# Kernel optimization log

Hardware: AMD Instinct MI355X
Metric: run time of the kernel (lower is better)

Reference implementation:

```python
import jax, jax.numpy as jnp
import numpy as np
from jax import lax

DN_CONV = ('NCHW', 'OIHW', 'NCHW')
DN_DECONV = ('NCHW', 'IOHW', 'NCHW')


def _conv(x, w, b, stride, pad):
    y = lax.conv_general_dilated(x, w, (stride, stride), ((pad, pad), (pad, pad)),
                                 dimension_numbers=DN_CONV)
    return y + b[None, :, None, None]


def _deconv(x, w, b):
    # torch ConvTranspose2d(k=4, stride=2, padding=1): equivalent to conv with
    # lhs_dilation=2, padding=k-1-p=2, spatially flipped kernel, weight [Cin,Cout,kH,kW].
    wf = w[:, :, ::-1, ::-1]
    y = lax.conv_general_dilated(x, wf, (1, 1), ((2, 2), (2, 2)),
                                 lhs_dilation=(2, 2), dimension_numbers=DN_DECONV)
    return y + b[None, :, None, None]


def setup_inputs() -> dict:
    key = jax.random.key(0)
    ks = jax.random.split(key, 14)
    s = 0.05
    H, D, K = 128, 64, 512  # hidden, embedding_dim, num_embeddings
    inp = {
        'x': jax.random.normal(ks[0], (32, 3, 256, 256), jnp.float32),
        'enc_w1': jax.random.normal(ks[1], (H, 3, 4, 4), jnp.float32) * s,
        'enc_b1': jnp.zeros((H,), jnp.float32),
        'enc_w2': jax.random.normal(ks[2], (H, H, 4, 4), jnp.float32) * s,
        'enc_b2': jnp.zeros((H,), jnp.float32),
        'enc_w3': jax.random.normal(ks[3], (D, H, 3, 3), jnp.float32) * s,
        'enc_b3': jnp.zeros((D,), jnp.float32),
        'codebook': jax.random.uniform(ks[4], (K, D), jnp.float32, -1.0 / K, 1.0 / K),
        'dec_w1': jax.random.normal(ks[5], (H, D, 3, 3), jnp.float32) * s,
        'dec_b1': jnp.zeros((H,), jnp.float32),
        'dec_w2': jax.random.normal(ks[6], (H, H, 4, 4), jnp.float32) * s,  # [Cin,Cout,4,4]
        'dec_b2': jnp.zeros((H,), jnp.float32),
        'dec_w3': jax.random.normal(ks[7], (H, 3, 4, 4), jnp.float32) * s,  # [Cin,Cout,4,4]
        'dec_b3': jnp.zeros((3,), jnp.float32),
    }
    return inp


def reference(x, enc_w1, enc_b1, enc_w2, enc_b2, enc_w3, enc_b3, codebook,
              dec_w1, dec_b1, dec_w2, dec_b2, dec_w3, dec_b3):
    # encoder
    h = jax.nn.relu(_conv(x, enc_w1, enc_b1, 2, 1))
    h = jax.nn.relu(_conv(h, enc_w2, enc_b2, 2, 1))
    z_e = _conv(h, enc_w3, enc_b3, 1, 1)  # [B, D, 64, 64]

    # vector quantization (faithful to torch .view(-1, D) memory reshape)
    D = codebook.shape[1]
    flat = z_e.reshape(-1, D)  # [N, D]
    d2 = (jnp.sum(flat * flat, axis=1, keepdims=True)
          + jnp.sum(codebook * codebook, axis=1)
          - 2.0 * flat @ codebook.T)  # [N, K]
    idx = jnp.argmin(d2, axis=1)
    z_q = jnp.take(codebook, idx, axis=0).reshape(z_e.shape)

    # decoder
    h = jax.nn.relu(_conv(z_q, dec_w1, dec_b1, 1, 1))
    h = jax.nn.relu(_deconv(h, dec_w2, dec_b2))
    x_recon = _deconv(h, dec_w3, dec_b3)
    return (x_recon, z_e, z_q)
```

## Files before the change

kernel.cpp:

```cpp
#include <hip/hip_runtime.h>
#include <hip/hip_bf16.h>


typedef unsigned short u16;
typedef unsigned int u32;
typedef unsigned long long u64;
typedef __attribute__((ext_vector_type(8))) short short8;
typedef __attribute__((ext_vector_type(4))) float f32x4;

__device__ __forceinline__ float bf2f(u16 u) {
    union { u32 i; float f; } x; x.i = ((u32)u) << 16; return x.f;
}
__device__ __forceinline__ u16 f2bf(float f) {
    __hip_bfloat16 h = __float2bfloat16(f);
    return *reinterpret_cast<u16*>(&h);
}

__global__ void g_k3(const float* __restrict__ w, u16* __restrict__ wg,
                     int CIN, int COUT)
{
    int idx = blockIdx.x * 256 + threadIdx.x;
    if (idx >= 9 * CIN * COUT) return;
    int ci = idx % CIN;
    int co = (idx / CIN) % COUT;
    int s  = idx / (CIN * COUT);
    wg[idx] = f2bf(w[(co * CIN + ci) * 9 + s]);
}

__global__ void g_enc2(const float* __restrict__ w, u16* __restrict__ wg)
{
    int idx = blockIdx.x * 256 + threadIdx.x;
    int ci = idx & 127, co = (idx >> 7) & 127, s = (idx >> 14) & 3, p = idx >> 16;
    int a = p >> 1, b = p & 1, j = s >> 1, i = s & 1;
    int ky = (1 - a) + 2 * j, kx = (1 - b) + 2 * i;
    wg[idx] = f2bf(w[((co << 7 | ci) << 4) + ky * 4 + kx]);
}

__global__ void g_dec2(const float* __restrict__ w, u16* __restrict__ wg)
{
    int idx = blockIdx.x * 256 + threadIdx.x;
    int ci = idx & 127, co = (idx >> 7) & 127, s = (idx >> 14) & 3, p = idx >> 16;
    int py = p >> 1, px = p & 1, j = s >> 1, i = s & 1;
    wg[idx] = f2bf(w[((ci << 7 | co) << 4) + (3 - (py + 2 * j)) * 4 + (3 - (px + 2 * i))]);
}

__global__ void g_dec3m(const float* __restrict__ w, u16* __restrict__ wg)
{
    int idx = blockIdx.x * 256 + threadIdx.x;
    if (idx >= 18432) return;
    int ci  = idx & 127;
    int row = (idx >> 7) & 15;
    int t   = idx >> 11;
    int dy = t / 3 - 1, dx = t % 3 - 1;
    float v = 0.f;
    if (row < 12) {
        int p = row / 3, co = row % 3;
        int py = p >> 1, px = p & 1;
        int a = dy + 1 - py, b2 = dx + 1 - px;
        if (a >= 0 && a <= 1 && b2 >= 0 && b2 <= 1)
            v = w[((ci * 3 + co) * 4 + (3 - (py + 2 * a))) * 4 + (3 - (px + 2 * b2))];
    }
    wg[idx] = f2bf(v);
}

__global__ void g_enc1(const float* __restrict__ w, u16* __restrict__ wg)
{
    int idx = blockIdx.x * 256 + threadIdx.x;
    if (idx >= 8192) return;
    int ci = idx & 3, kx = (idx >> 2) & 3, ky = (idx >> 4) & 3, co = idx >> 6;
    float v = 0.f;
    if (ci < 3) v = w[((co * 3 + ci) * 4 + ky) * 4 + kx];
    wg[idx] = f2bf(v);
}

__global__ void g_cbk(const float* __restrict__ cbk, u16* __restrict__ cb,
                      float* __restrict__ cn)
{
    int idx = blockIdx.x * 256 + threadIdx.x;
    if (idx >= 32768) return;
    cb[idx] = f2bf(cbk[idx]);
    if (idx < 512) {
        float s = 0.f;
        const float* r = cbk + idx * 64;
        for (int i = 0; i < 64; i++) s += r[i] * r[i];
        cn[idx] = s;
    }
}

__global__ __launch_bounds__(256) void xcl_k(
    const float* __restrict__ x, u16* __restrict__ xcl)
{
    const int y = blockIdx.x % 258, n = blockIdx.x / 258;
    const int gy = y - 1;
    for (int xx = threadIdx.x; xx < 258; xx += 256) {
        const int gx = xx - 1;
        u16 pk[4] = {0, 0, 0, 0};
        if (gy >= 0 && gy < 256 && gx >= 0 && gx < 256) {
            const size_t base = ((size_t)n * 3 * 256 + gy) * 256 + gx;
            pk[0] = f2bf(x[base]);
            pk[1] = f2bf(x[base + 65536]);
            pk[2] = f2bf(x[base + 131072]);
        }
        *(u64*)(xcl + ((size_t)(n * 258 + y) * 258 + xx) * 4) = *(const u64*)pk;
    }
}

__global__ __launch_bounds__(256) void enc1m_k(
    const u16* __restrict__ xcl, const u16* __restrict__ wg,
    const float* __restrict__ bias, u16* __restrict__ P)
{
    const int tid = threadIdx.x;
    const int l = tid & 63, w = tid >> 6;
    const int ln = l & 15, kg = l >> 4;
    const int px = w >> 1, half = w & 1;

    const int oy = blockIdx.x & 127;
    const int n  = blockIdx.x >> 7;
    const int p  = (oy & 1) * 2 + px;
    const int yy = oy >> 1;

    short8 af[8][2];
#pragma unroll
    for (int u = 0; u < 8; u++)
#pragma unroll
        for (int s = 0; s < 2; s++)
            af[u][s] = *(const short8*)(wg + ((u * 16 + ln) << 6) + s * 32 + 8 * kg);

    const u16* xn = xcl + (size_t)n * 258 * 258 * 4;
    const int r0 = 2 * oy;

#pragma unroll
    for (int t = 0; t < 2; t++) {
        const int xq = half * 32 + t * 16 + ln;
        const int ox = px + 2 * xq;

        short8 bf[2];
#pragma unroll
        for (int s = 0; s < 2; s++) {
            const int row = r0 + 2 * s + (kg >> 1);
            bf[s] = *(const short8*)(xn + ((size_t)row * 258 + 2 * ox) * 4
                                     + (kg & 1) * 8);
        }

        f32x4 acc[8];
#pragma unroll
        for (int u = 0; u < 8; u++) acc[u] = (f32x4){0.f, 0.f, 0.f, 0.f};
#pragma unroll
        for (int u = 0; u < 8; u++) {
            acc[u] = __builtin_amdgcn_mfma_f32_16x16x32_bf16(af[u][0], bf[0], acc[u], 0, 0, 0);
            acc[u] = __builtin_amdgcn_mfma_f32_16x16x32_bf16(af[u][1], bf[1], acc[u], 0, 0, 0);
        }

#pragma unroll
        for (int u = 0; u < 8; u++) {
            const int cobase = u * 16 + 4 * kg;
            u16 pk[4];
#pragma unroll
            for (int r = 0; r < 4; r++)
                pk[r] = f2bf(fmaxf(acc[u][r] + bias[cobase + r], 0.f));
            *(u64*)(P + ((((size_t)(n * 4 + p) * 64 + yy) * 64 + xq) << 7) + cobase)
                = *(const u64*)pk;
        }
    }
}

template<int J, int I, int NP, int NCW, int CI, int OUTM>
__global__ __launch_bounds__(512) void conv_mx3(
    const u16* __restrict__ x, const u16* __restrict__ wg,
    const float* __restrict__ bias, void* __restrict__ yv,
    int COUT)
{
    constexpr int G = 8 / NCW;
    constexpr int RS = 2 * G + 2;
    constexpr int TASKS = RS * 68 * 4;
    constexpr int SLOTS = (TASKS + 511) / 512;
    constexpr int CHP = CI / 32;
    constexpr int NCHUNK = NP * CHP;
    __shared__ u16 XL[RS * 68 * 40];

    const int tid = threadIdx.x;
    const int l = tid & 63, wv = tid >> 6;
    const int kg = l >> 4, ln = l & 15;
    const int cw = wv % NCW, g = wv / NCW;

    int b = blockIdx.x;
    constexpr int TILES = 64 / (2 * G);
    const int tile = b % TILES;  b /= TILES;
    const int n = b;
    const int OY0 = tile * (2 * G);

    bool valid[SLOTS], okm[SLOTS];
    int goff[SLOTS], loff[SLOTS];
#pragma unroll
    for (int s = 0; s < SLOTS; s++) {
        const int idx = s * 512 + tid;
        valid[s] = idx < TASKS;
        const int q = idx & 3, cc = (idx >> 2) % 68, r = (idx >> 2) / 68;
        const int gr = OY0 - 1 + r, gx = cc - 1;
        okm[s] = valid[s] && gr >= 0 && gr < 64 && gx >= 0 && gx < 64;
        goff[s] = okm[s] ? ((gr * 64 + gx) * CI + 8 * q) : 0;
        loff[s] = (r * 68 + cc) * 40 + 8 * q;
    }

    f32x4 acc[2][8];
#pragma unroll
    for (int u = 0; u < 2; u++)
#pragma unroll
        for (int t = 0; t < 8; t++) acc[u][t] = (f32x4){0.f, 0.f, 0.f, 0.f};

    const u16* xn = x + (size_t)n * NP * CI * 4096;
    const int co0 = cw * 32 + ln;
    const short8 z8 = (short8){0, 0, 0, 0, 0, 0, 0, 0};

    short8 pf[SLOTS];
    {
        const u16* xp = xn;
#pragma unroll
        for (int s = 0; s < SLOTS; s++)
            pf[s] = okm[s] ? *(const short8*)(xp + goff[s]) : z8;
    }

    for (int c = 0; c < NCHUNK; c++) {
        __syncthreads();
#pragma unroll
        for (int s = 0; s < SLOTS; s++)
            if (valid[s]) *(short8*)(XL + loff[s]) = pf[s];
        __syncthreads();

        if (c + 1 < NCHUNK) {
            const int cn_ = c + 1;
            const u16* xp = xn + (size_t)(cn_ / CHP) * CI * 4096
                            + (cn_ % CHP) * 32;
#pragma unroll
            for (int s = 0; s < SLOTS; s++)
                pf[s] = okm[s] ? *(const short8*)(xp + goff[s]) : z8;
        }

        const int p = c / CHP;
        const int ci0 = (c % CHP) * 32;
        int dy0, dx0;
        const u16* wgp;
        if (NP == 4) {
            dy0 = -(p >> 1); dx0 = -(p & 1);
            wgp = wg + (size_t)p * J * I * COUT * CI;
        } else {
            dy0 = -1; dx0 = -1; wgp = wg;
        }

#define TAP_ROW(jv)                                                          \
        {                                                                    \
            short8 wf0[I], wf1[I];                                           \
            _Pragma("unroll")                                                \
            for (int i = 0; i < I; i++) {                                    \
                const size_t wb = ((size_t)((jv) * I + i) * COUT + co0)      \
                                  * CI + ci0 + 8 * kg;                       \
                wf0[i] = *(const short8*)(wgp + wb);                         \
                wf1[i] = *(const short8*)(wgp + wb + (size_t)16 * CI);       \
            }                                                                \
            _Pragma("unroll")                                                \
            for (int i = 0; i < I; i++) {                                    \
                _Pragma("unroll")                                            \
                for (int t = 0; t < 8; t++) {                                \
                    const int rf = (t >> 2) + 2 * g + dy0 + 1 + (jv);        \
                    const int cf = (t & 3) * 16 + ln + dx0 + 1 + i;          \
                    const short8 bf = *(const short8*)(                      \
                        XL + (rf * 68 + cf) * 40 + 8 * kg);                  \
                    acc[0][t] = __builtin_amdgcn_mfma_f32_16x16x32_bf16(     \
                        wf0[i], bf, acc[0][t], 0, 0, 0);                     \
                    acc[1][t] = __builtin_amdgcn_mfma_f32_16x16x32_bf16(     \
                        wf1[i], bf, acc[1][t], 0, 0, 0);                     \
                }                                                            \
            }                                                                \
        }

        if constexpr (J == 2) {
            TAP_ROW(0); TAP_ROW(1);
        } else {
            TAP_ROW(0); TAP_ROW(1); TAP_ROW(2);
        }
#undef TAP_ROW
    }

#pragma unroll
    for (int u = 0; u < 2; u++) {
        const int cob = cw * 32 + u * 16 + 4 * kg;
#pragma unroll
        for (int t = 0; t < 8; t++) {
            const int oy = OY0 + 2 * g + (t >> 2);
            const int ox = (t & 3) * 16 + ln;
            if constexpr (OUTM == 1) {
                float* out = (float*)yv;
#pragma unroll
                for (int rr = 0; rr < 4; rr++)
                    out[(((size_t)n * COUT + cob + rr) * 64 + oy) * 64 + ox]
                        = acc[u][t][rr] + bias[cob + rr];
            } else {
                u16 pk[4];
#pragma unroll
                for (int rr = 0; rr < 4; rr++)
                    pk[rr] = f2bf(fmaxf(acc[u][t][rr] + bias[cob + rr], 0.f));
                *(u64*)((u16*)yv + ((size_t)(n * 64 + oy) * 64 + ox) * COUT
                        + cob) = *(const u64*)pk;
            }
        }
    }
}

__global__ __launch_bounds__(512) void dec2f_k(
    const u16* __restrict__ x, const u16* __restrict__ wg,
    const float* __restrict__ bias, u16* __restrict__ y)
{
    constexpr int RS = 4;
    constexpr int TASKS = RS * 68 * 4;
    constexpr int SLOTS = 3;
    __shared__ u16 XL[RS * 68 * 40];
    __shared__ u16 LW[8 * 16 * 136];

    const int tid = threadIdx.x;
    const int l = tid & 63, wv = tid >> 6;
    const int kg = l >> 4, ln = l & 15;
    const int pc = wv & 3, ch = wv >> 2;
    const int py = pc >> 1, px = pc & 1;

    int b = blockIdx.x;
    const int tile = b & 31;  b >>= 5;
    const int n = b;
    const int OY0 = tile * 2;

    bool valid[SLOTS], okm[SLOTS];
    int goff[SLOTS], loff[SLOTS];
#pragma unroll
    for (int s = 0; s < SLOTS; s++) {
        const int idx = s * 512 + tid;
        valid[s] = idx < TASKS;
        const int q = idx & 3, cc = (idx >> 2) % 68, r = (idx >> 2) / 68;
        const int gr = OY0 - 1 + r, gx = cc - 1;
        okm[s] = valid[s] && gr >= 0 && gr < 64 && gx >= 0 && gx < 64;
        goff[s] = okm[s] ? ((gr * 64 + gx) * 128 + 8 * q) : 0;
        loff[s] = (r * 68 + cc) * 40 + 8 * q;
    }

    f32x4 acc[8][4];
#pragma unroll
    for (int u = 0; u < 8; u++)
#pragma unroll
        for (int t = 0; t < 4; t++) acc[u][t] = (f32x4){0.f, 0.f, 0.f, 0.f};

    const u16* xn = x + (size_t)n * 64 * 64 * 128;
    const short8 z8 = (short8){0, 0, 0, 0, 0, 0, 0, 0};
    const u16* wgp = wg + (size_t)pc * 4 * 128 * 128;

    short8 pf[SLOTS];
#pragma unroll
    for (int s = 0; s < SLOTS; s++)
        pf[s] = okm[s] ? *(const short8*)(xn + goff[s]) : z8;

    for (int c = 0; c < 4; c++) {
        __syncthreads();
#pragma unroll
        for (int s = 0; s < SLOTS; s++)
            if (valid[s]) *(short8*)(XL + loff[s]) = pf[s];
        __syncthreads();

        if (c < 3) {
            const u16* xp = xn + (c + 1) * 32;
#pragma unroll
            for (int s = 0; s < SLOTS; s++)
                pf[s] = okm[s] ? *(const short8*)(xp + goff[s]) : z8;
        }

        const int ci0 = c * 32;

        short8 B3[3][2][2];
#pragma unroll
        for (int rw = 0; rw < 3; rw++) {
            const int rf = py + rw;
#pragma unroll
            for (int cb = 0; cb < 2; cb++) {
                const int cf0 = ch * 32 + cb * 16 + ln + px;
#pragma unroll
                for (int sh = 0; sh < 2; sh++)
                    B3[rw][sh][cb] = *(const short8*)(
                        XL + (rf * 68 + cf0 + sh) * 40 + 8 * kg);
            }
        }

#pragma unroll
        for (int u = 0; u < 8; u++) {
            short8 wf[4];
#pragma unroll
            for (int s4 = 0; s4 < 4; s4++)
                wf[s4] = *(const short8*)(
                    wgp + ((size_t)s4 * 128 + u * 16 + ln) * 128 + ci0 + 8 * kg);
#pragma unroll
            for (int m = 0; m < 2; m++)
#pragma unroll
                for (int cb = 0; cb < 2; cb++)
#pragma unroll
                    for (int j = 0; j < 2; j++)
#pragma unroll
                        for (int i = 0; i < 2; i++)
                            acc[u][m * 2 + cb] =
                                __builtin_amdgcn_mfma_f32_16x16x32_bf16(
                                    wf[j * 2 + i], B3[m + j][i][cb],
                                    acc[u][m * 2 + cb], 0, 0, 0);
        }
    }

    u16* lw = LW + wv * 16 * 136;
    const int q4 = l >> 4, ln15 = l & 15;
#pragma unroll
    for (int t = 0; t < 4; t++) {
        const int m = t >> 1, cb = t & 1;
#pragma unroll
        for (int u = 0; u < 8; u++) {
            const int cob = u * 16 + 4 * kg;
            u16 pk[4];
#pragma unroll
            for (int rr = 0; rr < 4; rr++)
                pk[rr] = f2bf(fmaxf(acc[u][t][rr] + bias[cob + rr], 0.f));
            *(u64*)(lw + ln * 136 + cob) = *(const u64*)pk;
        }
        asm volatile("s_waitcnt lgkmcnt(0)" ::: "memory");
        __builtin_amdgcn_sched_barrier(0);
        const int OY = 2 * (OY0 + m) + py;
#pragma unroll
        for (int rr2 = 0; rr2 < 4; rr2++) {
            const int pos = rr2 * 4 + q4;
            const short8 v = *(const short8*)(lw + pos * 136 + ln15 * 8);
            const int ox = ch * 32 + cb * 16 + pos;
            const int OX = 2 * ox + px;
            *(short8*)(y + ((size_t)(n * 128 + OY) * 128 + OX) * 128 + ln15 * 8) = v;
        }
        asm volatile("s_waitcnt lgkmcnt(0)" ::: "memory");
        __builtin_amdgcn_sched_barrier(0);
    }
}

__global__ __launch_bounds__(256) void dec3m_k(
    const u16* __restrict__ A2, const u16* __restrict__ wg,
    const float* __restrict__ bias, float* __restrict__ out)
{
    const int tid = threadIdx.x;
    const int l = tid & 63, wvi = tid >> 6;
    const int ln = l & 15, kg = l >> 4;

    int b = blockIdx.x;
    const int mxT = b & 7;  b >>= 3;
    const int myT = b & 3;  b >>= 2;
    const int n = b;
    const int X0 = mxT * 16;
    const int MY0 = myT * 32 + wvi * 8;
    const int xx = X0 + ln;

    const short8 z8 = (short8){0, 0, 0, 0, 0, 0, 0, 0};

    f32x4 acc[8];
#pragma unroll
    for (int m = 0; m < 8; m++) acc[m] = (f32x4){0.f, 0.f, 0.f, 0.f};

    int xoff[3]; bool xok[3];
#pragma unroll
    for (int sh = 0; sh < 3; sh++) {
        const int xv = xx + sh - 1;
        xok[sh] = (xv >= 0) & (xv < 128);
        xoff[sh] = (xok[sh] ? xv : 0) << 7;
    }

    for (int ks = 0; ks < 4; ks++) {
        const int cio = ks * 32 + 8 * kg;

        short8 at[9];
#pragma unroll
        for (int t = 0; t < 9; t++)
            at[t] = *(const short8*)(wg + (((size_t)t * 16 + ln) << 7) + cio);

        short8 B[10][3];
#pragma unroll
        for (int r = 0; r < 10; r++) {
            const int yy = MY0 - 1 + r;
            const bool yok = (yy >= 0) & (yy < 128);
            const size_t rowb = ((size_t)(n * 128 + (yok ? yy : 0)) << 7 << 7);
#pragma unroll
            for (int sh = 0; sh < 3; sh++) {
                short8 v = *(const short8*)(A2 + rowb + xoff[sh] + cio);
                B[r][sh] = (yok & xok[sh]) ? v : z8;
            }
            if (r >= 2) {
                const int m = r - 2;
#pragma unroll
                for (int rr = 0; rr < 3; rr++)
#pragma unroll
                    for (int sh = 0; sh < 3; sh++)
                        acc[m] = __builtin_amdgcn_mfma_f32_16x16x32_bf16(
                            at[rr * 3 + sh], B[m + rr][sh], acc[m], 0, 0, 0);
            }
        }
    }

    if (kg < 3) {
#pragma unroll
        for (int m = 0; m < 8; m++) {
            const int my = MY0 + m;
#pragma unroll
            for (int rr = 0; rr < 4; rr++) {
                const int row = 4 * kg + rr;
                const int p = row / 3, co = row % 3;
                const int oy = 2 * my + (p >> 1);
                const int ox = 2 * xx + (p & 1);
                out[(((size_t)(n * 3 + co)) << 16) + oy * 256 + ox]
                    = acc[m][rr] + bias[co];
            }
        }
    }
}

__global__ __launch_bounds__(256) void vqm2_k(
    const float* __restrict__ ze, const u16* __restrict__ cb,
    const float* __restrict__ cn, const float* __restrict__ cbk,
    float* __restrict__ zq, u16* __restrict__ zqcl)
{
    __shared__ float CN[512];
    __shared__ int IDX[64];
    __shared__ u16 CLDS[64][66];
    const int tid = threadIdx.x;
    const int l = tid & 63, wvi = tid >> 6;
    const int ln = l & 15, kg = l >> 4;

    const int n = blockIdx.x >> 6, y = blockIdx.x & 63;

    for (int i = tid; i < 512; i += 256) CN[i] = cn[i];
    __syncthreads();

    short8 az[2];
#pragma unroll
    for (int ks = 0; ks < 2; ks++) {
        const float* zp = ze + ((size_t)(n * 64 + wvi * 16 + ln) * 64 + y) * 64
                          + ks * 32 + 8 * kg;
        short8 t;
#pragma unroll
        for (int j = 0; j < 8; j++) t[j] = (short)f2bf(zp[j]);
        az[ks] = t;
    }

    float bval[4] = {3.4e38f, 3.4e38f, 3.4e38f, 3.4e38f};
    int bidx[4] = {0, 0, 0, 0};
    for (int nt = 0; nt < 32; nt++) {
        const int code = nt * 16 + ln;
        const short8 b0 = *(const short8*)(cb + (size_t)code * 64 + 8 * kg);
        const short8 b1 = *(const short8*)(cb + (size_t)code * 64 + 32 + 8 * kg);
        f32x4 d = (f32x4){0.f, 0.f, 0.f, 0.f};
        d = __builtin_amdgcn_mfma_f32_16x16x32_bf16(az[0], b0, d, 0, 0, 0);
        d = __builtin_amdgcn_mfma_f32_16x16x32_bf16(az[1], b1, d, 0, 0, 0);
        const float cnv = CN[code];
#pragma unroll
        for (int r = 0; r < 4; r++) {
            const float dist = cnv - 2.f * d[r];
            if (dist < bval[r]) { bval[r] = dist; bidx[r] = code; }
        }
    }
#pragma unroll
    for (int off = 1; off < 16; off <<= 1) {
#pragma unroll
        for (int r = 0; r < 4; r++) {
            const float ov = __shfl_xor(bval[r], off);
            const int oi = __shfl_xor(bidx[r], off);
            if (ov < bval[r] || (ov == bval[r] && oi < bidx[r])) {
                bval[r] = ov; bidx[r] = oi;
            }
        }
    }
    if (ln == 0) {
#pragma unroll
        for (int r = 0; r < 4; r++) IDX[wvi * 16 + 4 * kg + r] = bidx[r];
    }
    __syncthreads();

    {
        const int ci = tid >> 2, ch4 = tid & 3;
        const int bi = IDX[ci];
        const float4* sp = (const float4*)(cbk + (size_t)bi * 64 + ch4 * 16);
        float4* dp = (float4*)(zq + ((size_t)(n * 64 + ci) * 64 + y) * 64 + ch4 * 16);
#pragma unroll
        for (int q = 0; q < 4; q++) dp[q] = sp[q];
    }

    for (int idx = tid; idx < 4096; idx += 256) {
        const int ci = idx >> 6, xx = idx & 63;
        CLDS[ci][xx] = cb[(size_t)IDX[ci] * 64 + xx];
    }
    __syncthreads();
    for (int idx = tid; idx < 4096; idx += 256) {
        const int xx = idx >> 6, ci = idx & 63;
        zqcl[(((size_t)(n * 64 + y) * 64 + xx) << 6) + ci] = CLDS[ci][xx];
    }
}

extern "C" void kernel_launch(void* const* d_in, const int* in_sizes, int n_in,
                              void* d_out, int out_size, void* d_ws, size_t ws_size,
                              hipStream_t stream)
{
    (void)in_sizes; (void)n_in; (void)out_size; (void)ws_size;

    const float* x   = (const float*)d_in[0];
    const float* ew1 = (const float*)d_in[1];
    const float* eb1 = (const float*)d_in[2];
    const float* ew2 = (const float*)d_in[3];
    const float* eb2 = (const float*)d_in[4];
    const float* ew3 = (const float*)d_in[5];
    const float* eb3 = (const float*)d_in[6];
    const float* cbk = (const float*)d_in[7];
    const float* dw1 = (const float*)d_in[8];
    const float* db1 = (const float*)d_in[9];
    const float* dw2 = (const float*)d_in[10];
    const float* db2 = (const float*)d_in[11];
    const float* dw3 = (const float*)d_in[12];
    const float* db3 = (const float*)d_in[13];

    u16* P    = (u16*)d_ws;
    u16* ZQCL = P;
    u16* A2   = P;
    u16* B = (u16*)((char*)d_ws + 134217728);
    u16* XCL = B;
    u16* Wg2 = (u16*)((char*)d_ws + 167772160);
    u16* Wg3 = Wg2 + 262144;
    u16* Wg4 = Wg3 + 73728;
    u16* Wg5 = Wg4 + 73728;
    u16* Wg6 = Wg5 + 262144;
    u16* CB  = Wg6 + 32768;
    u16* Wg1 = CB + 32768;
    float* CNg = (float*)(Wg1 + 8192);

    float* xr = (float*)d_out;
    float* ze = xr + (size_t)32 * 3 * 256 * 256;
    float* zq = ze + (size_t)32 * 64 * 64 * 64;

    g_enc1<<<32, 256, 0, stream>>>(ew1, Wg1);
    g_enc2<<<1024, 256, 0, stream>>>(ew2, Wg2);
    g_k3<<<288, 256, 0, stream>>>(ew3, Wg3, 128, 64);
    g_k3<<<288, 256, 0, stream>>>(dw1, Wg4, 64, 128);
    g_dec2<<<1024, 256, 0, stream>>>(dw2, Wg5);
    g_dec3m<<<72, 256, 0, stream>>>(dw3, Wg6);
    g_cbk<<<128, 256, 0, stream>>>(cbk, CB, CNg);

    xcl_k<<<32 * 258, 256, 0, stream>>>(x, XCL);
    enc1m_k<<<32 * 128, 256, 0, stream>>>(XCL, Wg1, eb1, P);
    conv_mx3<2, 2, 4, 4, 128, 0><<<32 * 16, 512, 0, stream>>>(P, Wg2, eb2, B, 128);
    conv_mx3<3, 3, 1, 2, 128, 1><<<32 * 8, 512, 0, stream>>>(B, Wg3, eb3, ze, 64);
    vqm2_k<<<2048, 256, 0, stream>>>(ze, CB, CNg, cbk, zq, ZQCL);
    conv_mx3<3, 3, 1, 4, 64, 0><<<32 * 16, 512, 0, stream>>>(ZQCL, Wg4, db1, B, 128);
    dec2f_k<<<1024, 512, 0, stream>>>(B, Wg5, db2, A2);
    dec3m_k<<<1024, 256, 0, stream>>>(A2, Wg6, db3, xr);
}
```

Baseline: 563.6 us.

## Split dec2f output channels across grid.y, double-buffer input LDS tile

The deconv-2 kernel now splits its 128 output channels into two halves using blockIdx.y, so each block holds half the accumulators (acc[4][4] instead of acc[8][4]) and the grid doubles. This lowers register pressure and should raise occupancy. The input LDS tile is double-buffered so the next chunk is written during compute with one barrier per iteration instead of two, and setprio is raised around the MFMA loop. The cost is that each input tile is loaded and staged twice, once per channel half.

```diff
diff --git a/kernel.cpp b/kernel.cpp
--- a/kernel.cpp
+++ b/kernel.cpp
@@ -311,10 +311,11 @@
     const float* __restrict__ bias, u16* __restrict__ y)
 {
     constexpr int RS = 4;
+    constexpr int BUF = RS * 68 * 40;
     constexpr int TASKS = RS * 68 * 4;
     constexpr int SLOTS = 3;
-    __shared__ u16 XL[RS * 68 * 40];
-    __shared__ u16 LW[8 * 16 * 136];
+    __shared__ u16 XL[2 * BUF];
+    __shared__ u16 LW[8 * 16 * 72];
 
     const int tid = threadIdx.x;
     const int l = tid & 63, wv = tid >> 6;
@@ -325,6 +326,7 @@
     int b = blockIdx.x;
     const int tile = b & 31;  b >>= 5;
     const int n = b;
+    const int ub = blockIdx.y;
     const int OY0 = tile * 2;
 
     bool valid[SLOTS], okm[SLOTS];
@@ -340,9 +342,9 @@
         loff[s] = (r * 68 + cc) * 40 + 8 * q;
     }
 
-    f32x4 acc[8][4];
-#pragma unroll
-    for (int u = 0; u < 8; u++)
+    f32x4 acc[4][4];
+#pragma unroll
+    for (int u = 0; u < 4; u++)
 #pragma unroll
         for (int t = 0; t < 4; t++) acc[u][t] = (f32x4){0.f, 0.f, 0.f, 0.f};
 
@@ -354,14 +356,12 @@
 #pragma unroll
     for (int s = 0; s < SLOTS; s++)
         pf[s] = okm[s] ? *(const short8*)(xn + goff[s]) : z8;
+#pragma unroll
+    for (int s = 0; s < SLOTS; s++)
+        if (valid[s]) *(short8*)(XL + loff[s]) = pf[s];
+    __syncthreads();
 
     for (int c = 0; c < 4; c++) {
-        __syncthreads();
-#pragma unroll
-        for (int s = 0; s < SLOTS; s++)
-            if (valid[s]) *(short8*)(XL + loff[s]) = pf[s];
-        __syncthreads();
-
         if (c < 3) {
             const u16* xp = xn + (c + 1) * 32;
 #pragma unroll
@@ -369,6 +369,7 @@
                 pf[s] = okm[s] ? *(const short8*)(xp + goff[s]) : z8;
         }
 
+        const u16* XLc = XL + (c & 1) * BUF;
         const int ci0 = c * 32;
 
         short8 B3[3][2][2];
@@ -381,17 +382,19 @@
 #pragma unroll
                 for (int sh = 0; sh < 2; sh++)
                     B3[rw][sh][cb] = *(const short8*)(
-                        XL + (rf * 68 + cf0 + sh) * 40 + 8 * kg);
+                        XLc + (rf * 68 + cf0 + sh) * 40 + 8 * kg);
             }
         }
 
-#pragma unroll
-        for (int u = 0; u < 8; u++) {
+        __builtin_amdgcn_s_setprio(1);
+#pragma unroll
+        for (int u = 0; u < 4; u++) {
             short8 wf[4];
 #pragma unroll
             for (int s4 = 0; s4 < 4; s4++)
                 wf[s4] = *(const short8*)(
-                    wgp + ((size_t)s4 * 128 + u * 16 + ln) * 128 + ci0 + 8 * kg);
+                    wgp + ((size_t)s4 * 128 + ub * 64 + u * 16 + ln) * 128
+                    + ci0 + 8 * kg);
 #pragma unroll
             for (int m = 0; m < 2; m++)
 #pragma unroll
@@ -405,32 +408,41 @@
                                     wf[j * 2 + i], B3[m + j][i][cb],
                                     acc[u][m * 2 + cb], 0, 0, 0);
         }
-    }
-
-    u16* lw = LW + wv * 16 * 136;
-    const int q4 = l >> 4, ln15 = l & 15;
+        __builtin_amdgcn_s_setprio(0);
+
+        if (c < 3) {
+#pragma unroll
+            for (int s = 0; s < SLOTS; s++)
+                if (valid[s]) *(short8*)(XL + ((c + 1) & 1) * BUF + loff[s]) = pf[s];
+            __syncthreads();
+        }
+    }
+
+    u16* lw = LW + wv * 16 * 72;
 #pragma unroll
     for (int t = 0; t < 4; t++) {
         const int m = t >> 1, cb = t & 1;
 #pragma unroll
-        for (int u = 0; u < 8; u++) {
-            const int cob = u * 16 + 4 * kg;
+        for (int u = 0; u < 4; u++) {
+            const int cof = u * 16 + 4 * kg;
             u16 pk[4];
 #pragma unroll
             for (int rr = 0; rr < 4; rr++)
-                pk[rr] = f2bf(fmaxf(acc[u][t][rr] + bias[cob + rr], 0.f));
-            *(u64*)(lw + ln * 136 + cob) = *(const u64*)pk;
+                pk[rr] = f2bf(fmaxf(acc[u][t][rr] + bias[ub * 64 + cof + rr], 0.f));
+            *(u64*)(lw + ln * 72 + cof) = *(const u64*)pk;
         }
         asm volatile("s_waitcnt lgkmcnt(0)" ::: "memory");
         __builtin_amdgcn_sched_barrier(0);
         const int OY = 2 * (OY0 + m) + py;
 #pragma unroll
-        for (int rr2 = 0; rr2 < 4; rr2++) {
-            const int pos = rr2 * 4 + q4;
-            const short8 v = *(const short8*)(lw + pos * 136 + ln15 * 8);
+        for (int p2 = 0; p2 < 2; p2++) {
+            const int pos = p2 * 8 + (l >> 3);
+            const int ch8 = (l & 7) * 8;
+            const short8 v = *(const short8*)(lw + pos * 72 + ch8);
             const int ox = ch * 32 + cb * 16 + pos;
             const int OX = 2 * ox + px;
-            *(short8*)(y + ((size_t)(n * 128 + OY) * 128 + OX) * 128 + ln15 * 8) = v;
+            *(short8*)(y + ((size_t)(n * 128 + OY) * 128 + OX) * 128
+                       + ub * 64 + ch8) = v;
         }
         asm volatile("s_waitcnt lgkmcnt(0)" ::: "memory");
         __builtin_amdgcn_sched_barrier(0);
@@ -649,6 +661,6 @@
     conv_mx3<3, 3, 1, 2, 128, 1><<<32 * 8, 512, 0, stream>>>(B, Wg3, eb3, ze, 64);
     vqm2_k<<<2048, 256, 0, stream>>>(ze, CB, CNg, cbk, zq, ZQCL);
     conv_mx3<3, 3, 1, 4, 64, 0><<<32 * 16, 512, 0, stream>>>(ZQCL, Wg4, db1, B, 128);
-    dec2f_k<<<1024, 512, 0, stream>>>(B, Wg5, db2, A2);
+    dec2f_k<<<dim3(1024, 2), 512, 0, stream>>>(B, Wg5, db2, A2);
     dec3m_k<<<1024, 256, 0, stream>>>(A2, Wg6, db3, xr);
 }
```

New measurement: 572.9 us. No clear change (+1.6%).

## Double-buffer LDS input tiles in conv_mx3 to drop one barrier per chunk

Applied to the files above, without the earlier changes.

Adds a template flag that gives conv_mx3 two LDS buffers. The next chunk is stored into the alternate buffer while the current one is computed, and global prefetch runs two chunks ahead, so only one __syncthreads is needed per chunk instead of two. It is enabled for the enc2 and dec1 convolutions but not enc3. The cost is double the LDS footprint, which may lower occupancy, plus the `#pragma unroll 1` on the chunk loop.

```diff
diff --git a/kernel.cpp b/kernel.cpp
--- a/kernel.cpp
+++ b/kernel.cpp
@@ -164,7 +164,7 @@
     }
 }
 
-template<int J, int I, int NP, int NCW, int CI, int OUTM>
+template<int J, int I, int NP, int NCW, int CI, int OUTM, int DB>
 __global__ __launch_bounds__(512) void conv_mx3(
     const u16* __restrict__ x, const u16* __restrict__ wg,
     const float* __restrict__ bias, void* __restrict__ yv,
@@ -176,7 +176,8 @@
     constexpr int SLOTS = (TASKS + 511) / 512;
     constexpr int CHP = CI / 32;
     constexpr int NCHUNK = NP * CHP;
-    __shared__ u16 XL[RS * 68 * 40];
+    constexpr int BUF = RS * 68 * 40;
+    __shared__ u16 XL[(DB ? 2 : 1) * BUF];
 
     const int tid = threadIdx.x;
     const int l = tid & 63, wv = tid >> 6;
@@ -213,46 +214,34 @@
     const short8 z8 = (short8){0, 0, 0, 0, 0, 0, 0, 0};
 
     short8 pf[SLOTS];
-    {
-        const u16* xp = xn;
-#pragma unroll
-        for (int s = 0; s < SLOTS; s++)
-            pf[s] = okm[s] ? *(const short8*)(xp + goff[s]) : z8;
-    }
-
-    for (int c = 0; c < NCHUNK; c++) {
-        __syncthreads();
-#pragma unroll
-        for (int s = 0; s < SLOTS; s++)
-            if (valid[s]) *(short8*)(XL + loff[s]) = pf[s];
-        __syncthreads();
-
-        if (c + 1 < NCHUNK) {
-            const int cn_ = c + 1;
-            const u16* xp = xn + (size_t)(cn_ / CHP) * CI * 4096
-                            + (cn_ % CHP) * 32;
-#pragma unroll
-            for (int s = 0; s < SLOTS; s++)
-                pf[s] = okm[s] ? *(const short8*)(xp + goff[s]) : z8;
-        }
-
-        const int p = c / CHP;
-        const int ci0 = (c % CHP) * 32;
-        int dy0, dx0;
-        const u16* wgp;
-        if (NP == 4) {
-            dy0 = -(p >> 1); dx0 = -(p & 1);
-            wgp = wg + (size_t)p * J * I * COUT * CI;
-        } else {
-            dy0 = -1; dx0 = -1; wgp = wg;
-        }
-
-#define TAP_ROW(jv)                                                          \
-        {                                                                    \
+
+#define LOADCHUNK(cidx)                                                      \
+    {                                                                        \
+        const u16* xp = xn + (size_t)((cidx) / CHP) * CI * 4096              \
+                        + ((cidx) % CHP) * 32;                               \
+        _Pragma("unroll")                                                    \
+        for (int s = 0; s < SLOTS; s++)                                      \
+            pf[s] = okm[s] ? *(const short8*)(xp + goff[s]) : z8;            \
+    }
+
+#define COMPUTE_CHUNK(cvar, XLb)                                             \
+    {                                                                        \
+        const int p = (cvar) / CHP;                                          \
+        const int ci0 = ((cvar) % CHP) * 32;                                 \
+        int dy0, dx0;                                                        \
+        const u16* wgp;                                                      \
+        if (NP == 4) {                                                       \
+            dy0 = -(p >> 1); dx0 = -(p & 1);                                 \
+            wgp = wg + (size_t)p * J * I * COUT * CI;                        \
+        } else {                                                             \
+            dy0 = -1; dx0 = -1; wgp = wg;                                    \
+        }                                                                    \
+        _Pragma("unroll")                                                    \
+        for (int jv = 0; jv < J; jv++) {                                     \
             short8 wf0[I], wf1[I];                                           \
             _Pragma("unroll")                                                \
             for (int i = 0; i < I; i++) {                                    \
-                const size_t wb = ((size_t)((jv) * I + i) * COUT + co0)      \
+                const size_t wb = ((size_t)(jv * I + i) * COUT + co0)        \
                                   * CI + ci0 + 8 * kg;                       \
                 wf0[i] = *(const short8*)(wgp + wb);                         \
                 wf1[i] = *(const short8*)(wgp + wb + (size_t)16 * CI);       \
@@ -261,25 +250,54 @@
             for (int i = 0; i < I; i++) {                                    \
                 _Pragma("unroll")                                            \
                 for (int t = 0; t < 8; t++) {                                \
-                    const int rf = (t >> 2) + 2 * g + dy0 + 1 + (jv);        \
+                    const int rf = (t >> 2) + 2 * g + dy0 + 1 + jv;          \
                     const int cf = (t & 3) * 16 + ln + dx0 + 1 + i;          \
                     const short8 bf = *(const short8*)(                      \
-                        XL + (rf * 68 + cf) * 40 + 8 * kg);                  \
+                        (XLb) + (rf * 68 + cf) * 40 + 8 * kg);               \
                     acc[0][t] = __builtin_amdgcn_mfma_f32_16x16x32_bf16(     \
                         wf0[i], bf, acc[0][t], 0, 0, 0);                     \
                     acc[1][t] = __builtin_amdgcn_mfma_f32_16x16x32_bf16(     \
                         wf1[i], bf, acc[1][t], 0, 0, 0);                     \
                 }                                                            \
             }                                                                \
-        }
-
-        if constexpr (J == 2) {
-            TAP_ROW(0); TAP_ROW(1);
-        } else {
-            TAP_ROW(0); TAP_ROW(1); TAP_ROW(2);
-        }
-#undef TAP_ROW
-    }
+        }                                                                    \
+    }
+
+    if constexpr (DB) {
+        LOADCHUNK(0);
+#pragma unroll
+        for (int s = 0; s < SLOTS; s++)
+            if (valid[s]) *(short8*)(XL + loff[s]) = pf[s];
+        if (NCHUNK > 1) LOADCHUNK(1);
+
+#pragma unroll 1
+        for (int c = 0; c < NCHUNK; c++) {
+            __syncthreads();
+            if (c + 1 < NCHUNK) {
+#pragma unroll
+                for (int s = 0; s < SLOTS; s++)
+                    if (valid[s])
+                        *(short8*)(XL + ((c + 1) & 1) * BUF + loff[s]) = pf[s];
+            }
+            if (c + 2 < NCHUNK) LOADCHUNK(c + 2);
+            const u16* XLb = XL + (c & 1) * BUF;
+            COMPUTE_CHUNK(c, XLb);
+        }
+    } else {
+        LOADCHUNK(0);
+#pragma unroll 1
+        for (int c = 0; c < NCHUNK; c++) {
+            __syncthreads();
+#pragma unroll
+            for (int s = 0; s < SLOTS; s++)
+                if (valid[s]) *(short8*)(XL + loff[s]) = pf[s];
+            __syncthreads();
+            if (c + 1 < NCHUNK) LOADCHUNK(c + 1);
+            COMPUTE_CHUNK(c, XL);
+        }
+    }
+#undef LOADCHUNK
+#undef COMPUTE_CHUNK
 
 #pragma unroll
     for (int u = 0; u < 2; u++) {
@@ -645,10 +663,10 @@
 
     xcl_k<<<32 * 258, 256, 0, stream>>>(x, XCL);
     enc1m_k<<<32 * 128, 256, 0, stream>>>(XCL, Wg1, eb1, P);
-    conv_mx3<2, 2, 4, 4, 128, 0><<<32 * 16, 512, 0, stream>>>(P, Wg2, eb2, B, 128);
-    conv_mx3<3, 3, 1, 2, 128, 1><<<32 * 8, 512, 0, stream>>>(B, Wg3, eb3, ze, 64);
+    conv_mx3<2, 2, 4, 4, 128, 0, 1><<<32 * 16, 512, 0, stream>>>(P, Wg2, eb2, B, 128);
+    conv_mx3<3, 3, 1, 2, 128, 1, 0><<<32 * 8, 512, 0, stream>>>(B, Wg3, eb3, ze, 64);
     vqm2_k<<<2048, 256, 0, stream>>>(ze, CB, CNg, cbk, zq, ZQCL);
-    conv_mx3<3, 3, 1, 4, 64, 0><<<32 * 16, 512, 0, stream>>>(ZQCL, Wg4, db1, B, 128);
+    conv_mx3<3, 3, 1, 4, 64, 0, 1><<<32 * 16, 512, 0, stream>>>(ZQCL, Wg4, db1, B, 128);
     dec2f_k<<<1024, 512, 0, stream>>>(B, Wg5, db2, A2);
     dec3m_k<<<1024, 256, 0, stream>>>(A2, Wg6, db3, xr);
 }
```

Result: no change. 565.6 us (+0.4%).
